# Performance work log

Hardware: AMD Instinct MI355X
Metric: run time of the kernel (lower is better)

Reference implementation:

```python
import jax, jax.numpy as jnp
import numpy as np

S = 3072      # total tokens across all images
DIM = 1280    # hidden_size
H = 16        # num_heads
HD = DIM // H # head_dim = 80
NSEG = 6      # number of images (cu_seqlens has NSEG+1 entries)


def _rotate_half(x):
    x1, x2 = jnp.split(x, 2, axis=-1)
    return jnp.concatenate([-x2, x1], axis=-1)


def setup_inputs() -> dict:
    key = jax.random.key(0)
    ks = jax.random.split(key, 12)
    hidden_states = jax.random.normal(ks[0], (S, DIM), jnp.float32)
    # realistic vision rotary embedding: half-dim inv_freq, repeated to head_dim
    inv_freq = 1.0 / (10000.0 ** (jnp.arange(0, HD // 2, dtype=jnp.float32) / (HD // 2)))
    freqs = jnp.arange(S, dtype=jnp.float32)[:, None] * inv_freq[None, :]  # [S, HD/2]
    emb = jnp.concatenate([freqs, freqs], axis=-1)  # [S, HD]
    cos = jnp.cos(emb)
    sin = jnp.sin(emb)
    sc = 0.02
    wq = jax.random.normal(ks[1], (DIM, DIM), jnp.float32) * sc
    bq = jax.random.normal(ks[2], (DIM,), jnp.float32) * sc
    wk = jax.random.normal(ks[3], (DIM, DIM), jnp.float32) * sc
    bk = jax.random.normal(ks[4], (DIM,), jnp.float32) * sc
    wv = jax.random.normal(ks[5], (DIM, DIM), jnp.float32) * sc
    bv = jax.random.normal(ks[6], (DIM,), jnp.float32) * sc
    wo = jax.random.normal(ks[7], (DIM, DIM), jnp.float32) * sc
    bo = jax.random.normal(ks[8], (DIM,), jnp.float32) * sc
    cu_seqlens = (jnp.arange(NSEG + 1, dtype=jnp.int32) * (S // NSEG))  # [0,512,...,3072]
    return dict(hidden_states=hidden_states, cos=cos, sin=sin,
                wq=wq, bq=bq, wk=wk, bk=bk, wv=wv, bv=bv, wo=wo, bo=bo,
                cu_seqlens=cu_seqlens)


def reference(hidden_states, cos, sin, wq, bq, wk, bk, wv, bv, wo, bo, cu_seqlens):
    seq_length = hidden_states.shape[0]
    scaling = HD ** (-0.5)
    # QKV projections (torch Linear: x @ W.T + b)
    q = (hidden_states @ wq.T + bq).reshape(seq_length, H, HD)
    k = (hidden_states @ wk.T + bk).reshape(seq_length, H, HD)
    v = (hidden_states @ wv.T + bv).reshape(seq_length, H, HD)
    # apply_rotary_pos_emb_vision: cos/sin [S, HD] broadcast over head axis
    c = cos[:, None, :]
    s = sin[:, None, :]
    q = q * c + _rotate_half(q) * s
    k = k * c + _rotate_half(k) * s
    # block-diagonal (per-image) attention via segment mask
    seg = jnp.searchsorted(cu_seqlens[1:], jnp.arange(seq_length), side='right')
    mask = seg[:, None] == seg[None, :]  # [S, S] bool
    scores = jnp.einsum('shd,thd->hst', q, k) * scaling  # [H, S, S]
    scores = jnp.where(mask[None, :, :], scores, jnp.finfo(scores.dtype).min)
    attn = jax.nn.softmax(scores, axis=-1)
    out = jnp.einsum('hst,thd->shd', attn, v).reshape(seq_length, DIM)
    return out @ wo.T + bo
```

## Files before the change

kernel.cpp:

```cpp
#include <hip/hip_runtime.h>
#include <hip/hip_bf16.h>
#include <hip/hip_fp16.h>
#include <cstdint>
#include <cstddef>

typedef _Float16 f16;
typedef f16 f16x2 __attribute__((ext_vector_type(2)));
typedef f16 f16x4 __attribute__((ext_vector_type(4)));
typedef f16 f16x8 __attribute__((ext_vector_type(8)));
typedef float f32x4 __attribute__((ext_vector_type(4)));

#define S_LEN 3072
#define DIM 1280
#define NH 16
#define HD 80
#define SEG 512

#define MFMA16F(a, b, c) __builtin_amdgcn_mfma_f32_16x16x32_f16((a), (b), (c), 0, 0, 0)

__device__ __forceinline__ void gl2lds16(const void* g, void* l) {
    __builtin_amdgcn_global_load_lds(
        (const __attribute__((address_space(1))) unsigned int*)g,
        (__attribute__((address_space(3))) unsigned int*)l, 16, 0, 0);
}

__device__ __forceinline__ unsigned int pack2(float a, float b) {
    f16x2 t = {(f16)a, (f16)b};
    union { f16x2 v; unsigned int u; } c;
    c.v = t;
    return c.u;
}

__global__ __launch_bounds__(256) void cvt_kernel(
    const float* __restrict__ hs,
    const float* __restrict__ wq, const float* __restrict__ wk,
    const float* __restrict__ wv, const float* __restrict__ wo,
    f16* __restrict__ hs16,
    f16* __restrict__ wq16, f16* __restrict__ wk16,
    f16* __restrict__ wv16, f16* __restrict__ wo16)
{
    const int m = blockIdx.y;
    const float* src; f16* dst; int n4;
    if (m == 0)      { src = hs; dst = hs16; n4 = S_LEN * DIM / 4; }
    else if (m == 1) { src = wq; dst = wq16; n4 = DIM * DIM / 4; }
    else if (m == 2) { src = wk; dst = wk16; n4 = DIM * DIM / 4; }
    else if (m == 3) { src = wv; dst = wv16; n4 = DIM * DIM / 4; }
    else             { src = wo; dst = wo16; n4 = DIM * DIM / 4; }
    int idx = blockIdx.x * 256 + threadIdx.x;
    if (idx >= n4) return;
    f32x4 v = *(const f32x4*)(src + (size_t)idx * 4);
    f16x4 o;
#pragma unroll
    for (int e = 0; e < 4; ++e) o[e] = (f16)v[e];
    *(f16x4*)(dst + (size_t)idx * 4) = o;
}

__global__ __launch_bounds__(256) void gemm_f16_kernel(
    const f16* __restrict__ A,
    const f16* __restrict__ W0, const f16* __restrict__ W1, const f16* __restrict__ W2,
    const float* __restrict__ b0, const float* __restrict__ b1, const float* __restrict__ b2,
    f16* __restrict__ O0, f16* __restrict__ O1, f16* __restrict__ O2,
    float* __restrict__ OF, int mode_base)
{
    const int mode = mode_base + blockIdx.z;
    const f16* W = (mode == 1) ? W1 : (mode == 2) ? W2 : W0;
    const float* bias = (mode == 1) ? b1 : (mode == 2) ? b2 : b0;

    __shared__ __align__(16) f16 As[128 * 32];
    __shared__ __align__(16) f16 Bs[128 * 32];

    const int tid = threadIdx.x;
    const int lane = tid & 63;
    const int lane15 = tid & 15;
    const int quad = lane >> 4;
    const int w = tid >> 6;
    const int wm = (w >> 1) * 64;
    const int wn = (w & 1) * 64;
    const int m0 = blockIdx.x * 128;
    const int n0 = blockIdx.y * 128;

    const int srow = w * 32 + (lane >> 2);
    const int scol = (lane & 3) * 8;
    const f16* gA0 = A + (size_t)(m0 + srow) * DIM + scol;
    const f16* gA1 = A + (size_t)(m0 + srow + 16) * DIM + scol;
    const f16* gB0 = W + (size_t)(n0 + srow) * DIM + scol;
    const f16* gB1 = W + (size_t)(n0 + srow + 16) * DIM + scol;
    f16* lA0 = As + (w * 32) * 32;
    f16* lA1 = As + (w * 32 + 16) * 32;
    f16* lB0 = Bs + (w * 32) * 32;
    f16* lB1 = Bs + (w * 32 + 16) * 32;

    f32x4 acc[4][4];
#pragma unroll
    for (int i = 0; i < 4; ++i)
#pragma unroll
        for (int j = 0; j < 4; ++j)
            acc[i][j] = (f32x4){0.f, 0.f, 0.f, 0.f};

    for (int kt = 0; kt < DIM / 32; ++kt) {
        __syncthreads();
        gl2lds16(gA0 + kt * 32, lA0);
        gl2lds16(gA1 + kt * 32, lA1);
        gl2lds16(gB0 + kt * 32, lB0);
        gl2lds16(gB1 + kt * 32, lB1);
        __syncthreads();

        f16x8 fa[4], fb[4];
#pragma unroll
        for (int i = 0; i < 4; ++i)
            fa[i] = *(const f16x8*)(As + (wm + i * 16 + lane15) * 32 + quad * 8);
#pragma unroll
        for (int j = 0; j < 4; ++j)
            fb[j] = *(const f16x8*)(Bs + (wn + j * 16 + lane15) * 32 + quad * 8);
#pragma unroll
        for (int i = 0; i < 4; ++i)
#pragma unroll
            for (int j = 0; j < 4; ++j)
                acc[i][j] = MFMA16F(fa[i], fb[j], acc[i][j]);
    }

    float bvv[4];
#pragma unroll
    for (int j = 0; j < 4; ++j)
        bvv[j] = bias[n0 + wn + j * 16 + lane15];

    if (mode == 3) {
#pragma unroll
        for (int i = 0; i < 4; ++i)
#pragma unroll
            for (int j = 0; j < 4; ++j)
#pragma unroll
                for (int r = 0; r < 4; ++r) {
                    int row = m0 + wm + i * 16 + quad * 4 + r;
                    int col = n0 + wn + j * 16 + lane15;
                    OF[(size_t)row * DIM + col] = acc[i][j][r] + bvv[j];
                }
    } else {
        f16* O = (mode == 0) ? O0 : (mode == 1) ? O1 : O2;
#pragma unroll
        for (int i = 0; i < 4; ++i)
#pragma unroll
            for (int j = 0; j < 4; ++j)
#pragma unroll
                for (int r = 0; r < 4; ++r) {
                    int row = m0 + wm + i * 16 + quad * 4 + r;
                    int col = n0 + wn + j * 16 + lane15;
                    O[(size_t)row * DIM + col] = (f16)(acc[i][j][r] + bvv[j]);
                }
    }
}

__global__ __launch_bounds__(256) void vtrans_kernel(
    const f16* __restrict__ v, f16* __restrict__ vT)
{
    const int h = blockIdx.x;
    const int s0 = blockIdx.y * 128;
    __shared__ __align__(16) f16 Ls[128 * 128];
    const int tid = threadIdx.x;
#pragma unroll
    for (int c = tid; c < 1280; c += 256) {
        int r = c / 10;
        int ch = c - r * 10;
        int chs = ch ^ ((r >> 3) & 7);
        *(f16x8*)(Ls + r * 128 + chs * 8) =
            *(const f16x8*)(v + (size_t)(s0 + r) * DIM + h * HD + ch * 8);
    }
    __syncthreads();
#pragma unroll
    for (int c = tid; c < 1280; c += 256) {
        int d = c >> 4;
        int sc = c & 15;
        f16x8 ov;
#pragma unroll
        for (int e = 0; e < 8; ++e) {
            int s = sc * 8 + e;
            ov[e] = Ls[s * 128 + (((d >> 3) ^ (sc & 7)) * 8) + (d & 7)];
        }
        *(f16x8*)(vT + (size_t)(h * HD + d) * S_LEN + s0 + sc * 8) = ov;
    }
}

__global__ __launch_bounds__(256) void rope_kernel(
    f16* __restrict__ qb, f16* __restrict__ kb,
    const float* __restrict__ cosb, const float* __restrict__ sinb)
{
    int idx = blockIdx.x * 256 + threadIdx.x;
    int c = idx % 5;
    int t = idx / 5;
    int h = t & 15; t >>= 4;
    int s = t % S_LEN;
    int which = t / S_LEN;
    f16* buf = which ? kb : qb;
    float scale = which ? 1.0f : 0.11180339887498948f;
    int j = c * 8;
    f32x4 ca = *(const f32x4*)(cosb + s * HD + j);
    f32x4 cb = *(const f32x4*)(cosb + s * HD + j + 4);
    f32x4 sna = *(const f32x4*)(sinb + s * HD + j);
    f32x4 snb = *(const f32x4*)(sinb + s * HD + j + 4);
    size_t base = (size_t)s * DIM + h * HD + j;
    f16x8 x1 = *(f16x8*)(buf + base);
    f16x8 x2 = *(f16x8*)(buf + base + 40);
    f16x8 o1, o2;
#pragma unroll
    for (int e = 0; e < 8; ++e) {
        float ce = (e < 4) ? ca[e] : cb[e - 4];
        float se = (e < 4) ? sna[e] : snb[e - 4];
        float a = (float)x1[e], b = (float)x2[e];
        o1[e] = (f16)((a * ce - b * se) * scale);
        o2[e] = (f16)((b * ce + a * se) * scale);
    }
    *(f16x8*)(buf + base) = o1;
    *(f16x8*)(buf + base + 40) = o2;
}

__global__ __launch_bounds__(256) void attn_kernel(
    const f16* __restrict__ q, const f16* __restrict__ k,
    const f16* __restrict__ vT, f16* __restrict__ o)
{
    const int h = blockIdx.x;
    const int g = blockIdx.y;
    const int qc = blockIdx.z;
    const int tid = threadIdx.x;
    const int lane15 = tid & 15;
    const int quad = (tid & 63) >> 4;
    const int w = tid >> 6;
    const int qbase = g * SEG + qc * 64;
    const int qrow = qbase + w * 16 + lane15;

    __shared__ __align__(16) f16 Ks[128 * 88];
    __shared__ __align__(16) f16 Vt[80 * 128];

    f16x8 zf;
#pragma unroll
    for (int e = 0; e < 8; ++e) zf[e] = (f16)0.0f;

    f16x8 fq[3];
#pragma unroll
    for (int kc = 0; kc < 3; ++kc) {
        if (kc == 2 && quad >= 2) fq[kc] = zf;
        else fq[kc] = *(const f16x8*)(q + (size_t)qrow * DIM + h * HD + kc * 32 + quad * 8);
    }

    float m_run = -1e30f, l_run = 0.f;
    f32x4 Oa[5];
#pragma unroll
    for (int dt = 0; dt < 5; ++dt) Oa[dt] = (f32x4){0.f, 0.f, 0.f, 0.f};

    for (int kt = 0; kt < 4; ++kt) {
        __syncthreads();
        const int kb = g * SEG + kt * 128;
#pragma unroll
        for (int c = tid; c < 1280; c += 256) {
            int r = c / 10;
            int c8 = (c - r * 10) * 8;
            *(f16x8*)(Ks + r * 88 + c8) =
                *(const f16x8*)(k + (size_t)(kb + r) * DIM + h * HD + c8);
        }
#pragma unroll
        for (int c = tid; c < 1280; c += 256) {
            int d = c >> 4;
            int sc = c & 15;
            *(f16x8*)(Vt + d * 128 + (sc ^ (d & 7)) * 8) =
                *(const f16x8*)(vT + (size_t)(h * HD + d) * S_LEN + kb + sc * 8);
        }
        __syncthreads();

        f32x4 sa[8];
#pragma unroll
        for (int nt = 0; nt < 8; ++nt) sa[nt] = (f32x4){0.f, 0.f, 0.f, 0.f};
#pragma unroll
        for (int kc = 0; kc < 3; ++kc) {
#pragma unroll
            for (int nt = 0; nt < 8; ++nt) {
                f16x8 fk;
                if (kc == 2 && quad >= 2) fk = zf;
                else fk = *(const f16x8*)(Ks + (nt * 16 + lane15) * 88 + kc * 32 + quad * 8);
                sa[nt] = MFMA16F(fk, fq[kc], sa[nt]);
            }
        }

        float mt = -1e30f;
#pragma unroll
        for (int nt = 0; nt < 8; ++nt)
#pragma unroll
            for (int r = 0; r < 4; ++r) mt = fmaxf(mt, sa[nt][r]);
        mt = fmaxf(mt, __shfl_xor(mt, 16, 64));
        mt = fmaxf(mt, __shfl_xor(mt, 32, 64));

        float mn = fmaxf(m_run, mt);
        float alpha = __expf(m_run - mn);
        m_run = mn;
        float lt = 0.f;
        unsigned int pp[8][2];
#pragma unroll
        for (int nt = 0; nt < 8; ++nt) {
            float p0 = __expf(sa[nt][0] - mn);
            float p1 = __expf(sa[nt][1] - mn);
            float p2 = __expf(sa[nt][2] - mn);
            float p3 = __expf(sa[nt][3] - mn);
            lt += (p0 + p1) + (p2 + p3);
            pp[nt][0] = pack2(p0, p1);
            pp[nt][1] = pack2(p2, p3);
        }
        lt += __shfl_xor(lt, 16, 64);
        lt += __shfl_xor(lt, 32, 64);
        l_run = l_run * alpha + lt;

#pragma unroll
        for (int dt = 0; dt < 5; ++dt)
#pragma unroll
            for (int r = 0; r < 4; ++r) Oa[dt][r] *= alpha;

        const int srcA = ((quad & 1) * 2) * 16 + lane15;
        const int srcB = srcA + 16;
        const bool hi = quad >= 2;
#pragma unroll
        for (int kc2 = 0; kc2 < 4; ++kc2) {
            unsigned int e0 = __shfl((int)pp[2 * kc2][0], srcA, 64);
            unsigned int e1 = __shfl((int)pp[2 * kc2][1], srcA, 64);
            unsigned int e2 = __shfl((int)pp[2 * kc2][0], srcB, 64);
            unsigned int e3 = __shfl((int)pp[2 * kc2][1], srcB, 64);
            unsigned int o0 = __shfl((int)pp[2 * kc2 + 1][0], srcA, 64);
            unsigned int o1 = __shfl((int)pp[2 * kc2 + 1][1], srcA, 64);
            unsigned int o2 = __shfl((int)pp[2 * kc2 + 1][0], srcB, 64);
            unsigned int o3 = __shfl((int)pp[2 * kc2 + 1][1], srcB, 64);
            union { unsigned int u[4]; f16x8 v; } fp;
            fp.u[0] = hi ? o0 : e0;
            fp.u[1] = hi ? o1 : e1;
            fp.u[2] = hi ? o2 : e2;
            fp.u[3] = hi ? o3 : e3;
#pragma unroll
            for (int dt = 0; dt < 5; ++dt) {
                int drow = dt * 16 + lane15;
                int slot = (kc2 * 4 + quad) ^ (drow & 7);
                f16x8 fv = *(const f16x8*)(Vt + drow * 128 + slot * 8);
                Oa[dt] = MFMA16F(fv, fp.v, Oa[dt]);
            }
        }
    }

    float inv = 1.0f / l_run;
#pragma unroll
    for (int dt = 0; dt < 5; ++dt) {
        f16x4 ov;
#pragma unroll
        for (int r = 0; r < 4; ++r) ov[r] = (f16)(Oa[dt][r] * inv);
        *(f16x4*)(o + (size_t)qrow * DIM + h * HD + dt * 16 + quad * 4) = ov;
    }
}

extern "C" void kernel_launch(void* const* d_in, const int* in_sizes, int n_in,
                              void* d_out, int out_size, void* d_ws, size_t ws_size,
                              hipStream_t stream)
{
    const float* hs   = (const float*)d_in[0];
    const float* cosb = (const float*)d_in[1];
    const float* sinb = (const float*)d_in[2];
    const float* wq   = (const float*)d_in[3];
    const float* bq   = (const float*)d_in[4];
    const float* wk   = (const float*)d_in[5];
    const float* bk   = (const float*)d_in[6];
    const float* wv   = (const float*)d_in[7];
    const float* bv   = (const float*)d_in[8];
    const float* wo   = (const float*)d_in[9];
    const float* bo   = (const float*)d_in[10];

    const size_t SD = (size_t)S_LEN * DIM;
    const size_t WW = (size_t)DIM * DIM;
    f16* hs16 = (f16*)d_ws;
    f16* wq16 = hs16 + SD;
    f16* wk16 = wq16 + WW;
    f16* wv16 = wk16 + WW;
    f16* wo16 = wv16 + WW;
    f16* q16  = wo16 + WW;
    f16* k16  = q16 + SD;
    f16* v16  = k16 + SD;
    f16* ao16 = v16 + SD;
    f16* vT16 = ao16 + SD;
    float* outb = (float*)d_out;

    cvt_kernel<<<dim3(S_LEN * DIM / 4 / 256, 5), 256, 0, stream>>>(
        hs, wq, wk, wv, wo, hs16, wq16, wk16, wv16, wo16);
    gemm_f16_kernel<<<dim3(24, 10, 3), 256, 0, stream>>>(
        hs16, wq16, wk16, wv16, bq, bk, bv, q16, k16, v16, nullptr, 0);
    vtrans_kernel<<<dim3(NH, 24), 256, 0, stream>>>(v16, vT16);
    rope_kernel<<<1920, 256, 0, stream>>>(q16, k16, cosb, sinb);
    attn_kernel<<<dim3(NH, 6, 8), 256, 0, stream>>>(q16, k16, vT16, ao16);
    gemm_f16_kernel<<<dim3(24, 10, 1), 256, 0, stream>>>(
        ao16, wo16, nullptr, nullptr, bo, nullptr, nullptr,
        nullptr, nullptr, nullptr, outb, 3);
}
```

Before: 226.3 us.

## Merge rope and V-transpose kernels; use smaller tiles for output projection GEMM

The rope and V-transpose kernels become one launch that dispatches on block index, which saves one kernel launch and its gap. The output projection gets its own GEMM kernel with 64x128 tiles, giving 480 blocks instead of 240 so the GPU's many CUs are better filled. The trade-off is a higher global load per FLOP for the smaller tiles, and the merged kernel reserves 32KB of LDS even for the rope blocks, which could lower their occupancy.

```diff
diff --git a/kernel.cpp b/kernel.cpp
--- a/kernel.cpp
+++ b/kernel.cpp
@@ -59,10 +59,9 @@
     const f16* __restrict__ A,
     const f16* __restrict__ W0, const f16* __restrict__ W1, const f16* __restrict__ W2,
     const float* __restrict__ b0, const float* __restrict__ b1, const float* __restrict__ b2,
-    f16* __restrict__ O0, f16* __restrict__ O1, f16* __restrict__ O2,
-    float* __restrict__ OF, int mode_base)
-{
-    const int mode = mode_base + blockIdx.z;
+    f16* __restrict__ O0, f16* __restrict__ O1, f16* __restrict__ O2)
+{
+    const int mode = blockIdx.z;
     const f16* W = (mode == 1) ? W1 : (mode == 2) ? W2 : W0;
     const float* bias = (mode == 1) ? b1 : (mode == 2) ? b2 : b0;
 
@@ -124,93 +123,151 @@
     for (int j = 0; j < 4; ++j)
         bvv[j] = bias[n0 + wn + j * 16 + lane15];
 
-    if (mode == 3) {
+    f16* O = (mode == 0) ? O0 : (mode == 1) ? O1 : O2;
+#pragma unroll
+    for (int i = 0; i < 4; ++i)
+#pragma unroll
+        for (int j = 0; j < 4; ++j)
+#pragma unroll
+            for (int r = 0; r < 4; ++r) {
+                int row = m0 + wm + i * 16 + quad * 4 + r;
+                int col = n0 + wn + j * 16 + lane15;
+                O[(size_t)row * DIM + col] = (f16)(acc[i][j][r] + bvv[j]);
+            }
+}
+
+__global__ __launch_bounds__(256) void gemm_out_kernel(
+    const f16* __restrict__ A, const f16* __restrict__ W,
+    const float* __restrict__ bias, float* __restrict__ OF)
+{
+    __shared__ __align__(16) f16 As[64 * 32];
+    __shared__ __align__(16) f16 Bs[128 * 32];
+
+    const int tid = threadIdx.x;
+    const int lane = tid & 63;
+    const int lane15 = tid & 15;
+    const int quad = lane >> 4;
+    const int w = tid >> 6;
+    const int wn = w * 32;
+    const int m0 = blockIdx.x * 64;
+    const int n0 = blockIdx.y * 128;
+
+    const int srA = w * 16 + (lane >> 2);
+    const int srB = w * 32 + (lane >> 2);
+    const int scol = (lane & 3) * 8;
+    const f16* gA0 = A + (size_t)(m0 + srA) * DIM + scol;
+    const f16* gB0 = W + (size_t)(n0 + srB) * DIM + scol;
+    const f16* gB1 = W + (size_t)(n0 + srB + 16) * DIM + scol;
+    f16* lA0 = As + (w * 16) * 32;
+    f16* lB0 = Bs + (w * 32) * 32;
+    f16* lB1 = Bs + (w * 32 + 16) * 32;
+
+    f32x4 acc[4][2];
+#pragma unroll
+    for (int i = 0; i < 4; ++i)
+#pragma unroll
+        for (int j = 0; j < 2; ++j)
+            acc[i][j] = (f32x4){0.f, 0.f, 0.f, 0.f};
+
+    for (int kt = 0; kt < DIM / 32; ++kt) {
+        __syncthreads();
+        gl2lds16(gA0 + kt * 32, lA0);
+        gl2lds16(gB0 + kt * 32, lB0);
+        gl2lds16(gB1 + kt * 32, lB1);
+        __syncthreads();
+
+        f16x8 fa[4], fb[2];
 #pragma unroll
         for (int i = 0; i < 4; ++i)
-#pragma unroll
-            for (int j = 0; j < 4; ++j)
-#pragma unroll
-                for (int r = 0; r < 4; ++r) {
-                    int row = m0 + wm + i * 16 + quad * 4 + r;
-                    int col = n0 + wn + j * 16 + lane15;
-                    OF[(size_t)row * DIM + col] = acc[i][j][r] + bvv[j];
-                }
-    } else {
-        f16* O = (mode == 0) ? O0 : (mode == 1) ? O1 : O2;
+            fa[i] = *(const f16x8*)(As + (i * 16 + lane15) * 32 + quad * 8);
+#pragma unroll
+        for (int j = 0; j < 2; ++j)
+            fb[j] = *(const f16x8*)(Bs + (wn + j * 16 + lane15) * 32 + quad * 8);
 #pragma unroll
         for (int i = 0; i < 4; ++i)
 #pragma unroll
-            for (int j = 0; j < 4; ++j)
-#pragma unroll
-                for (int r = 0; r < 4; ++r) {
-                    int row = m0 + wm + i * 16 + quad * 4 + r;
-                    int col = n0 + wn + j * 16 + lane15;
-                    O[(size_t)row * DIM + col] = (f16)(acc[i][j][r] + bvv[j]);
-                }
-    }
-}
-
-__global__ __launch_bounds__(256) void vtrans_kernel(
+            for (int j = 0; j < 2; ++j)
+                acc[i][j] = MFMA16F(fa[i], fb[j], acc[i][j]);
+    }
+
+    float bvv[2];
+#pragma unroll
+    for (int j = 0; j < 2; ++j)
+        bvv[j] = bias[n0 + wn + j * 16 + lane15];
+
+#pragma unroll
+    for (int i = 0; i < 4; ++i)
+#pragma unroll
+        for (int j = 0; j < 2; ++j)
+#pragma unroll
+            for (int r = 0; r < 4; ++r) {
+                int row = m0 + i * 16 + quad * 4 + r;
+                int col = n0 + wn + j * 16 + lane15;
+                OF[(size_t)row * DIM + col] = acc[i][j][r] + bvv[j];
+            }
+}
+
+__global__ __launch_bounds__(256) void prep_kernel(
+    f16* __restrict__ qb, f16* __restrict__ kb,
+    const float* __restrict__ cosb, const float* __restrict__ sinb,
     const f16* __restrict__ v, f16* __restrict__ vT)
 {
-    const int h = blockIdx.x;
-    const int s0 = blockIdx.y * 128;
     __shared__ __align__(16) f16 Ls[128 * 128];
     const int tid = threadIdx.x;
-#pragma unroll
-    for (int c = tid; c < 1280; c += 256) {
-        int r = c / 10;
-        int ch = c - r * 10;
-        int chs = ch ^ ((r >> 3) & 7);
-        *(f16x8*)(Ls + r * 128 + chs * 8) =
-            *(const f16x8*)(v + (size_t)(s0 + r) * DIM + h * HD + ch * 8);
-    }
-    __syncthreads();
-#pragma unroll
-    for (int c = tid; c < 1280; c += 256) {
-        int d = c >> 4;
-        int sc = c & 15;
-        f16x8 ov;
+    if (blockIdx.x < 1920) {
+        int idx = blockIdx.x * 256 + tid;
+        int c = idx % 5;
+        int t = idx / 5;
+        int h = t & 15; t >>= 4;
+        int s = t % S_LEN;
+        int which = t / S_LEN;
+        f16* buf = which ? kb : qb;
+        float scale = which ? 1.0f : 0.11180339887498948f;
+        int j = c * 8;
+        f32x4 ca = *(const f32x4*)(cosb + s * HD + j);
+        f32x4 cb = *(const f32x4*)(cosb + s * HD + j + 4);
+        f32x4 sna = *(const f32x4*)(sinb + s * HD + j);
+        f32x4 snb = *(const f32x4*)(sinb + s * HD + j + 4);
+        size_t base = (size_t)s * DIM + h * HD + j;
+        f16x8 x1 = *(f16x8*)(buf + base);
+        f16x8 x2 = *(f16x8*)(buf + base + 40);
+        f16x8 o1, o2;
 #pragma unroll
         for (int e = 0; e < 8; ++e) {
-            int s = sc * 8 + e;
-            ov[e] = Ls[s * 128 + (((d >> 3) ^ (sc & 7)) * 8) + (d & 7)];
-        }
-        *(f16x8*)(vT + (size_t)(h * HD + d) * S_LEN + s0 + sc * 8) = ov;
-    }
-}
-
-__global__ __launch_bounds__(256) void rope_kernel(
-    f16* __restrict__ qb, f16* __restrict__ kb,
-    const float* __restrict__ cosb, const float* __restrict__ sinb)
-{
-    int idx = blockIdx.x * 256 + threadIdx.x;
-    int c = idx % 5;
-    int t = idx / 5;
-    int h = t & 15; t >>= 4;
-    int s = t % S_LEN;
-    int which = t / S_LEN;
-    f16* buf = which ? kb : qb;
-    float scale = which ? 1.0f : 0.11180339887498948f;
-    int j = c * 8;
-    f32x4 ca = *(const f32x4*)(cosb + s * HD + j);
-    f32x4 cb = *(const f32x4*)(cosb + s * HD + j + 4);
-    f32x4 sna = *(const f32x4*)(sinb + s * HD + j);
-    f32x4 snb = *(const f32x4*)(sinb + s * HD + j + 4);
-    size_t base = (size_t)s * DIM + h * HD + j;
-    f16x8 x1 = *(f16x8*)(buf + base);
-    f16x8 x2 = *(f16x8*)(buf + base + 40);
-    f16x8 o1, o2;
-#pragma unroll
-    for (int e = 0; e < 8; ++e) {
-        float ce = (e < 4) ? ca[e] : cb[e - 4];
-        float se = (e < 4) ? sna[e] : snb[e - 4];
-        float a = (float)x1[e], b = (float)x2[e];
-        o1[e] = (f16)((a * ce - b * se) * scale);
-        o2[e] = (f16)((b * ce + a * se) * scale);
-    }
-    *(f16x8*)(buf + base) = o1;
-    *(f16x8*)(buf + base + 40) = o2;
+            float ce = (e < 4) ? ca[e] : cb[e - 4];
+            float se = (e < 4) ? sna[e] : snb[e - 4];
+            float a = (float)x1[e], b = (float)x2[e];
+            o1[e] = (f16)((a * ce - b * se) * scale);
+            o2[e] = (f16)((b * ce + a * se) * scale);
+        }
+        *(f16x8*)(buf + base) = o1;
+        *(f16x8*)(buf + base + 40) = o2;
+    } else {
+        int bid = blockIdx.x - 1920;
+        const int h = bid / 24;
+        const int s0 = (bid - h * 24) * 128;
+#pragma unroll
+        for (int c = tid; c < 1280; c += 256) {
+            int r = c / 10;
+            int ch = c - r * 10;
+            int chs = ch ^ ((r >> 3) & 7);
+            *(f16x8*)(Ls + r * 128 + chs * 8) =
+                *(const f16x8*)(v + (size_t)(s0 + r) * DIM + h * HD + ch * 8);
+        }
+        __syncthreads();
+#pragma unroll
+        for (int c = tid; c < 1280; c += 256) {
+            int d = c >> 4;
+            int sc = c & 15;
+            f16x8 ov;
+#pragma unroll
+            for (int e = 0; e < 8; ++e) {
+                int s = sc * 8 + e;
+                ov[e] = Ls[s * 128 + (((d >> 3) ^ (sc & 7)) * 8) + (d & 7)];
+            }
+            *(f16x8*)(vT + (size_t)(h * HD + d) * S_LEN + s0 + sc * 8) = ov;
+        }
+    }
 }
 
 __global__ __launch_bounds__(256) void attn_kernel(
@@ -382,11 +439,8 @@
     cvt_kernel<<<dim3(S_LEN * DIM / 4 / 256, 5), 256, 0, stream>>>(
         hs, wq, wk, wv, wo, hs16, wq16, wk16, wv16, wo16);
     gemm_f16_kernel<<<dim3(24, 10, 3), 256, 0, stream>>>(
-        hs16, wq16, wk16, wv16, bq, bk, bv, q16, k16, v16, nullptr, 0);
-    vtrans_kernel<<<dim3(NH, 24), 256, 0, stream>>>(v16, vT16);
-    rope_kernel<<<1920, 256, 0, stream>>>(q16, k16, cosb, sinb);
+        hs16, wq16, wk16, wv16, bq, bk, bv, q16, k16, v16);
+    prep_kernel<<<2304, 256, 0, stream>>>(q16, k16, cosb, sinb, v16, vT16);
     attn_kernel<<<dim3(NH, 6, 8), 256, 0, stream>>>(q16, k16, vT16, ao16);
-    gemm_f16_kernel<<<dim3(24, 10, 1), 256, 0, stream>>>(
-        ao16, wo16, nullptr, nullptr, bo, nullptr, nullptr,
-        nullptr, nullptr, nullptr, outb, 3);
-}
+    gemm_out_kernel<<<dim3(48, 10), 256, 0, stream>>>(ao16, wo16, bo, outb);
+}
```

After: 219.3 us. 1.03x faster.
